# Kernel optimization log

Measured on AMD Instinct MI355X. Metric: run time of the kernel, lower is better.

## Reference

```python
import jax, jax.numpy as jnp
import numpy as np

CUTOFF = 5.0          # module init kwarg
N_BASIS = 64
PI_HALF = np.pi / 2.0  # self.pi_half buffer, the C parameter in the formula


def setup_inputs() -> dict:
    key = jax.random.key(0)
    k1, k2 = jax.random.split(key)
    N, box = 2048, 10.0
    # per-point scalar feature (density-like, positive)
    f = jax.random.uniform(k1, (N, 1), dtype=jnp.float32)
    # 3D coordinates in a box; cutoff=5.0 so the Step mask is nontrivial
    coords = jax.random.uniform(k2, (N, 3), dtype=jnp.float32) * box
    # buffers from __init__: means = linspace(0, cutoff, n_basis) / cutoff, beta = (scale*n_basis)^2
    means = jnp.linspace(0.0, CUTOFF, N_BASIS, dtype=jnp.float32) / CUTOFF
    beta = jnp.asarray(float(N_BASIS) ** 2, dtype=jnp.float32)
    return {"f": f, "coords": coords, "means": means, "beta": beta}


def reference(f, coords, means, beta):
    # forward: coords (and out_coords==coords) are divided by cutoff, so all
    # distances below are in normalized units and the cutoff is at d == 1.
    c = coords / CUTOFF                      # [N, 3]
    diff = c[:, None, :] - c[None, :, :]     # [N, M, 3]  (R_i - r_j)
    sq = jnp.sum(diff * diff, axis=-1)       # [N, M]
    d = jnp.sqrt(jnp.maximum(sq, 1e-12))     # Norm2(R - r), safe at d=0
    # Cos(C*d) * Step(1 - d) * F_j   -> scalar pair weight [N, M]
    w = jnp.cos(PI_HALF * d) * (d <= 1.0).astype(f.dtype) * f[:, 0][None, :]
    # Exp(-B * (d - M_b)^2)          -> Gaussian basis expansion [N, M, n_basis]
    g = jnp.exp(-beta * (d[..., None] - means) ** 2)
    # Sum reduction over j (axis=1 in Genred)
    return jnp.einsum('nm,nmb->nb', w, g)    # [N, n_basis]
```

## Files before the change

kernel.cpp:

```cpp
#include <hip/hip_runtime.h>
#include <math.h>

#define NB 64
#define BLOCK 256
#define WPB 4
#define NPTS_MAX 2048
#define CHUNKS 8

#if __has_builtin(__builtin_amdgcn_exp2f)
#define EXP2F(x) __builtin_amdgcn_exp2f(x)
#else
#define EXP2F(x) exp2f(x)
#endif
#if __has_builtin(__builtin_amdgcn_cosf)
#define COSREV(x) __builtin_amdgcn_cosf(x)
#else
#define COSREV(x) __cosf(6.28318530718f * (x))
#endif
#if __has_builtin(__builtin_amdgcn_sqrtf)
#define SQRTF(x) __builtin_amdgcn_sqrtf(x)
#else
#define SQRTF(x) sqrtf(x)
#endif

__global__ void __launch_bounds__(BLOCK, 6)
wgp_kernel(const float* __restrict__ f,
           const float* __restrict__ coords,
           const float* __restrict__ means,
           const float* __restrict__ beta,
           float* __restrict__ out,
           int n_pts) {
    __shared__ float2   sorted[NPTS_MAX];
    __shared__ unsigned hist[NB];
    __shared__ int      S[NB + 1];
    __shared__ float    red[WPB][NB];

    const int tid  = threadIdx.x;
    const int lane = tid & 63;
    const int wid  = tid >> 6;
    const int n    = blockIdx.x;

    const float xn = coords[3 * n + 0];
    const float yn = coords[3 * n + 1];
    const float zn = coords[3 * n + 2];
    const float kk = -1.44269504089f * beta[0];
    const float mu = means[lane];

    if (tid < NB) hist[tid] = 0u;
    __syncthreads();

    float dv[CHUNKS], wv[CHUNKS];
    int   kr[CHUNKS];
#pragma unroll
    for (int c = 0; c < CHUNKS; ++c) {
        const int m = c * BLOCK + tid;
        float d = 0.f, w = 0.f;
        int krc = -1;
        if (m < n_pts) {
            const float dx = xn - coords[3 * m + 0];
            const float dy = yn - coords[3 * m + 1];
            const float dz = zn - coords[3 * m + 2];
            const float sqn = fmaf(dx, dx, fmaf(dy, dy, dz * dz)) * 0.04f;
            d = SQRTF(fmaxf(sqn, 1e-12f));
            if (d <= 1.0f) {
                w = COSREV(0.25f * d) * f[m];
                int key = (int)fmaf(d, 63.0f, 0.5f);
                key = key > 63 ? 63 : key;
                const unsigned r = atomicAdd(&hist[key], 1u);
                krc = (key << 16) | (int)r;
            }
        }
        dv[c] = d; wv[c] = w; kr[c] = krc;
    }
    __syncthreads();

    if (wid == 0) {
        const unsigned v = hist[lane];
        unsigned incl = v;
#pragma unroll
        for (int s = 1; s < 64; s <<= 1) {
            const unsigned t = __shfl_up(incl, s, 64);
            if (lane >= s) incl += t;
        }
        S[lane + 1] = (int)incl;
        if (lane == 0) S[0] = 0;
    }
    __syncthreads();

#pragma unroll
    for (int c = 0; c < CHUNKS; ++c) {
        if (kr[c] >= 0) {
            const int key  = kr[c] >> 16;
            const int rank = kr[c] & 0xFFFF;
            sorted[S[key] + rank] = make_float2(dv[c], wv[c]);
        }
    }
    __syncthreads();

    const int bmin = lane > 4  ? lane - 4 : 0;
    const int bmax = lane < 59 ? lane + 4 : 63;
    const int lo0  = S[bmin];
    const int hi0  = S[bmax + 1];
    float acc = 0.f;
    int i = lo0 + ((wid - lo0) & 3);
#pragma unroll 2
    for (; i < hi0; i += 4) {
        const float2 p = sorted[i];
        const float t = p.x - mu;
        acc = fmaf(p.y, EXP2F(kk * (t * t)), acc);
    }

    red[wid][lane] = acc;
    __syncthreads();
    if (wid == 0) {
        out[n * NB + lane] = (red[0][lane] + red[1][lane])
                           + (red[2][lane] + red[3][lane]);
    }
}

extern "C" void kernel_launch(void* const* d_in, const int* in_sizes, int n_in,
                              void* d_out, int out_size, void* d_ws, size_t ws_size,
                              hipStream_t stream) {
    const float* f      = (const float*)d_in[0];
    const float* coords = (const float*)d_in[1];
    const float* means  = (const float*)d_in[2];
    const float* beta   = (const float*)d_in[3];
    float* out = (float*)d_out;

    const int n = in_sizes[0];
    wgp_kernel<<<n, BLOCK, 0, stream>>>(f, coords, means, beta, out, n);
}
```

Before: 75.49 us.

## Replace per-pair Gaussian evaluation with gridded moment binning and Taylor convolution

Instead of sorting neighbors by distance and evaluating exp for each neighbor-basis pair, each neighbor's weight is deposited into a fine grid (1008 bins) as zeroth, first and second moments via shared-memory float atomics. Each basis output is then computed as a fixed 145-tap convolution with precomputed Gaussian values and their first and second derivatives, using a second-order Taylor expansion. This removes the histogram, scan and scatter phases and decouples the output cost from neighbor count. In exchange it adds float atomic contention, a truncation approximation of the Gaussian tail and of the Taylor expansion, and nondeterministic summation order.

Measured after the change: 89.07 us. 18.0% more time.

```diff
diff --git a/kernel.cpp b/kernel.cpp
--- a/kernel.cpp
+++ b/kernel.cpp
@@ -4,8 +4,12 @@
 #define NB 64
 #define BLOCK 256
 #define WPB 4
-#define NPTS_MAX 2048
-#define CHUNKS 8
+#define KHALF 72
+#define NTAP (2 * KHALF + 1)
+#define QGUARD 5
+#define QLEN 76
+#define WSTRIDE (16 * QLEN)
+#define WTOT (3 * WSTRIDE)
 
 #if __has_builtin(__builtin_amdgcn_exp2f)
 #define EXP2F(x) __builtin_amdgcn_exp2f(x)
@@ -30,84 +34,74 @@
            const float* __restrict__ beta,
            float* __restrict__ out,
            int n_pts) {
-    __shared__ float2   sorted[NPTS_MAX];
-    __shared__ unsigned hist[NB];
-    __shared__ int      S[NB + 1];
-    __shared__ float    red[WPB][NB];
+    __shared__ float  W[WTOT];
+    __shared__ float4 A[NTAP];
+    __shared__ float  red[WPB][NB];
 
     const int tid  = threadIdx.x;
     const int lane = tid & 63;
     const int wid  = tid >> 6;
     const int n    = blockIdx.x;
 
+    float4* W4 = (float4*)W;
+#pragma unroll
+    for (int i = tid; i < WTOT / 4; i += BLOCK) W4[i] = make_float4(0.f, 0.f, 0.f, 0.f);
+
+    const float h      = 1.0f / 1008.0f;
+    const float beta_v = beta[0];
+    const float kk     = -1.44269504089f * beta_v;
+
+    if (tid < NTAP) {
+        const float u = (float)(tid - KHALF) * h;
+        const float E = EXP2F(kk * u * u);
+        A[tid] = make_float4(E,
+                             -2.0f * beta_v * u * E,
+                             (2.0f * beta_v * beta_v * u * u - beta_v) * E,
+                             0.0f);
+    }
+
     const float xn = coords[3 * n + 0];
     const float yn = coords[3 * n + 1];
     const float zn = coords[3 * n + 2];
-    const float kk = -1.44269504089f * beta[0];
-    const float mu = means[lane];
 
-    if (tid < NB) hist[tid] = 0u;
     __syncthreads();
 
-    float dv[CHUNKS], wv[CHUNKS];
-    int   kr[CHUNKS];
-#pragma unroll
-    for (int c = 0; c < CHUNKS; ++c) {
+    const int chunks = (n_pts + BLOCK - 1) / BLOCK;
+    for (int c = 0; c < chunks; ++c) {
         const int m = c * BLOCK + tid;
-        float d = 0.f, w = 0.f;
-        int krc = -1;
         if (m < n_pts) {
             const float dx = xn - coords[3 * m + 0];
             const float dy = yn - coords[3 * m + 1];
             const float dz = zn - coords[3 * m + 2];
             const float sqn = fmaf(dx, dx, fmaf(dy, dy, dz * dz)) * 0.04f;
-            d = SQRTF(fmaxf(sqn, 1e-12f));
+            const float d = SQRTF(fmaxf(sqn, 1e-12f));
             if (d <= 1.0f) {
-                w = COSREV(0.25f * d) * f[m];
-                int key = (int)fmaf(d, 63.0f, 0.5f);
-                key = key > 63 ? 63 : key;
-                const unsigned r = atomicAdd(&hist[key], 1u);
-                krc = (key << 16) | (int)r;
+                const float w  = COSREV(0.25f * d) * f[m];
+                const float jf = floorf(fmaf(d, 1008.0f, 0.5f));
+                const int   j  = (int)jf;
+                const float dl = fmaf(jf, -h, d);
+                const int   q  = (j >> 4) + QGUARD;
+                const int   r  = j & 15;
+                const int off  = r * QLEN + q;
+                atomicAdd(&W[off],               w);
+                atomicAdd(&W[WSTRIDE + off],     w * dl);
+                atomicAdd(&W[2 * WSTRIDE + off], w * dl * dl);
             }
-        }
-        dv[c] = d; wv[c] = w; kr[c] = krc;
-    }
-    __syncthreads();
-
-    if (wid == 0) {
-        const unsigned v = hist[lane];
-        unsigned incl = v;
-#pragma unroll
-        for (int s = 1; s < 64; s <<= 1) {
-            const unsigned t = __shfl_up(incl, s, 64);
-            if (lane >= s) incl += t;
-        }
-        S[lane + 1] = (int)incl;
-        if (lane == 0) S[0] = 0;
-    }
-    __syncthreads();
-
-#pragma unroll
-    for (int c = 0; c < CHUNKS; ++c) {
-        if (kr[c] >= 0) {
-            const int key  = kr[c] >> 16;
-            const int rank = kr[c] & 0xFFFF;
-            sorted[S[key] + rank] = make_float2(dv[c], wv[c]);
         }
     }
     __syncthreads();
 
-    const int bmin = lane > 4  ? lane - 4 : 0;
-    const int bmax = lane < 59 ? lane + 4 : 63;
-    const int lo0  = S[bmin];
-    const int hi0  = S[bmax + 1];
     float acc = 0.f;
-    int i = lo0 + ((wid - lo0) & 3);
-#pragma unroll 2
-    for (; i < hi0; i += 4) {
-        const float2 p = sorted[i];
-        const float t = p.x - mu;
-        acc = fmaf(p.y, EXP2F(kk * (t * t)), acc);
+#pragma unroll 1
+    for (int kidx = wid; kidx < NTAP; kidx += WPB) {
+        const float4 a = A[kidx];
+        const int jj  = 16 * lane + (kidx - KHALF);
+        const int q   = (jj >> 4) + QGUARD;
+        const int r   = jj & 15;
+        const int off = r * QLEN + q;
+        acc = fmaf(a.x, W[off],               acc);
+        acc = fmaf(a.y, W[WSTRIDE + off],     acc);
+        acc = fmaf(a.z, W[2 * WSTRIDE + off], acc);
     }
 
     red[wid][lane] = acc;
```
